# Kernel optimization log

Hardware: AMD Instinct MI355X
Metric: run time of the kernel (lower is better)

The kernel has to match this reference:

```python
import jax, jax.numpy as jnp
import numpy as np

INPUT_SIZE = 512
HIDDEN_SIZE = 512


def setup_inputs() -> dict:
    key = jax.random.key(0)
    k1, k2, k3, k4, k5 = jax.random.split(key, 5)
    B, N = 8, 2048
    x = jax.random.normal(k1, (B, N, INPUT_SIZE), dtype=jnp.float32)
    # Linear params (torch nn.Linear: y = x @ W^T + b), init scale ~ 1/sqrt(fan_in)
    s = 1.0 / np.sqrt(INPUT_SIZE)
    Wq = jax.random.uniform(k2, (HIDDEN_SIZE, INPUT_SIZE), minval=-s, maxval=s, dtype=jnp.float32)
    bq = jax.random.uniform(k3, (HIDDEN_SIZE,), minval=-s, maxval=s, dtype=jnp.float32)
    Wk = jax.random.uniform(k4, (HIDDEN_SIZE, INPUT_SIZE), minval=-s, maxval=s, dtype=jnp.float32)
    bk = jax.random.uniform(k5, (HIDDEN_SIZE,), minval=-s, maxval=s, dtype=jnp.float32)
    return {"x": x, "Wq": Wq, "bq": bq, "Wk": Wk, "bk": bk}


def reference(x, Wq, bq, Wk, bk):
    # q, k: [B, N, H]
    q = jnp.einsum('bnd,hd->bnh', x, Wq) + bq
    k = jnp.einsum('bnd,hd->bnh', x, Wk) + bk
    # scores: [B, N, N], softmax over last axis (dim=2)
    scores = jnp.einsum('bnh,bmh->bnm', q, k) / jnp.sqrt(jnp.float32(HIDDEN_SIZE))
    attn = jax.nn.softmax(scores, axis=2)
    # attended = attn^T @ x : [B, N, input_size]; squeeze(2) no-op since input_size>1
    attended = jnp.einsum('bnm,bnd->bmd', attn, x)
    return attended
```

## Files before the change

kernel.cpp:

```cpp
#include <hip/hip_runtime.h>

typedef __bf16 bf16x8 __attribute__((ext_vector_type(8)));
typedef __bf16 bf16x4 __attribute__((ext_vector_type(4)));
typedef float f32x4 __attribute__((ext_vector_type(4)));

__device__ __forceinline__ void async_copy16(const void* g, void* l) {
    __builtin_amdgcn_global_load_lds(
        (const __attribute__((address_space(1))) void*)g,
        (__attribute__((address_space(3))) void*)l, 16, 0, 0);
}

__global__ __launch_bounds__(256) void cvt_kernel(
    const float4* __restrict__ x, const float4* __restrict__ Wq,
    const float4* __restrict__ Wk, const float4* __restrict__ bq,
    const float4* __restrict__ bk,
    bf16x4* __restrict__ xb, bf16x4* __restrict__ Wb,
    float4* __restrict__ biasc) {
    int i = blockIdx.x * 256 + threadIdx.x;
    if (i < 2097152) {
        float4 v = x[i];
        bf16x4 r = {(__bf16)v.x, (__bf16)v.y, (__bf16)v.z, (__bf16)v.w};
        xb[i] = r;
    }
    if (i < 131072) {
        float4 v = (i < 65536) ? Wq[i] : Wk[i - 65536];
        bf16x4 r = {(__bf16)v.x, (__bf16)v.y, (__bf16)v.z, (__bf16)v.w};
        Wb[i] = r;
    }
    if (i < 256) {
        biasc[i] = (i < 128) ? bq[i] : bk[i - 128];
    }
}

__global__ __launch_bounds__(256) void fold_kernel(
    const __bf16* __restrict__ xb, const float* __restrict__ Z,
    ushort* __restrict__ xzT) {
    __shared__ float tile[64][65];
    __shared__ float zin[64];
    const int b = blockIdx.y;
    const int td = blockIdx.x & 7;
    const int tn = blockIdx.x >> 3;
    const int n0 = tn * 64, d0 = td * 64;
    const int t = threadIdx.x;
    if (t < 64) zin[t] = 1.0f / Z[b * 2048 + n0 + t];
    __syncthreads();
    const int cl = t & 15, c4 = cl * 4, rr = t >> 4;
#pragma unroll
    for (int j = 0; j < 4; ++j) {
        int nr = rr + j * 16;
        bf16x4 v = *(const bf16x4*)&xb[((size_t)b * 2048 + n0 + nr) * 512 + d0 + c4];
        tile[nr][c4 + 0] = (float)v[0];
        tile[nr][c4 + 1] = (float)v[1];
        tile[nr][c4 + 2] = (float)v[2];
        tile[nr][c4 + 3] = (float)v[3];
    }
    __syncthreads();
#pragma unroll
    for (int j2 = 0; j2 < 4; ++j2) {
        int dr = rr + j2 * 16;
        bf16x4 pk;
#pragma unroll
        for (int j = 0; j < 4; ++j)
            pk[j] = (__bf16)(tile[j * 16 + cl][dr] * zin[c4 + j]);
        *(bf16x4*)&xzT[((size_t)b * 512 + d0 + dr) * 2048 + n0 + c4] = pk;
    }
}

template <int EPI>
__global__ __launch_bounds__(256) void gemm_bt(
    const ushort* __restrict__ A, int lda, long sA,
    const ushort* __restrict__ B, int ldb, long sB,
    void* __restrict__ C, int ldc, long sC,
    int tiles_n, int K,
    const float* __restrict__ bias, float scale,
    float* __restrict__ Z, long sZ) {
    __shared__ ushort lA[128 * 64];
    __shared__ ushort lB[128 * 64];
    const int b = blockIdx.y;
    A += (size_t)b * sA;
    B += (size_t)b * sB;
    const int tm = blockIdx.x / tiles_n, tn = blockIdx.x % tiles_n;
    const int t = threadIdx.x;
    const int l = t & 63, w = t >> 6;
    const int wr = w >> 1, wc = w & 1;

    f32x4 acc[4][4];
#pragma unroll
    for (int i = 0; i < 4; ++i)
#pragma unroll
        for (int j = 0; j < 4; ++j) acc[i][j] = (f32x4){0.f, 0.f, 0.f, 0.f};

    for (int k0 = 0; k0 < K; k0 += 64) {
#pragma unroll
        for (int p = 0; p < 4; ++p) {
            int off = p * 4096 + t * 16;
            int row = off >> 7;
            int kb = off & 127;
            int kswz = kb ^ ((row & 7) << 4);
            async_copy16(A + (size_t)(tm * 128 + row) * lda + k0 + (kswz >> 1),
                         (char*)lA + off);
            async_copy16(B + (size_t)(tn * 128 + row) * ldb + k0 + (kswz >> 1),
                         (char*)lB + off);
        }
        __syncthreads();
#pragma unroll
        for (int ks = 0; ks < 2; ++ks) {
            bf16x8 af[4], bfr[4];
#pragma unroll
            for (int i = 0; i < 4; ++i) {
                int row = wr * 64 + i * 16 + (l & 15);
                int colb = (ks * 64 + (l >> 4) * 16) ^ ((row & 7) << 4);
                af[i] = *(const bf16x8*)((const char*)lA + row * 128 + colb);
            }
#pragma unroll
            for (int j = 0; j < 4; ++j) {
                int row = wc * 64 + j * 16 + (l & 15);
                int colb = (ks * 64 + (l >> 4) * 16) ^ ((row & 7) << 4);
                bfr[j] = *(const bf16x8*)((const char*)lB + row * 128 + colb);
            }
#pragma unroll
            for (int i = 0; i < 4; ++i)
#pragma unroll
                for (int j = 0; j < 4; ++j)
                    acc[i][j] = __builtin_amdgcn_mfma_f32_16x16x32_bf16(
                        af[i], bfr[j], acc[i][j], 0, 0, 0);
        }
        __syncthreads();
    }

    const int mb = tm * 128 + wr * 64;
    const int nb = tn * 128 + wc * 64;
    const int cl = l & 15;

    if (EPI == 0) {
        ushort* Cp = (ushort*)C + (size_t)b * sC;
#pragma unroll
        for (int i = 0; i < 4; ++i)
#pragma unroll
            for (int q = 0; q < 4; ++q) {
                int row = mb + i * 16 + (l >> 4) * 4 + q;
                bf16x4 pk;
#pragma unroll
                for (int j = 0; j < 4; ++j)
                    pk[j] = (__bf16)(acc[i][j][q] + bias[nb + j * 16 + cl]);
                *(bf16x4*)&Cp[(size_t)row * ldc + nb + cl * 4] = pk;
            }
    } else if (EPI == 1) {
        ushort* Cp = (ushort*)C + (size_t)b * sC;
        float colsum[4] = {0.f, 0.f, 0.f, 0.f};
#pragma unroll
        for (int i = 0; i < 4; ++i)
#pragma unroll
            for (int q = 0; q < 4; ++q) {
                int row = mb + i * 16 + (l >> 4) * 4 + q;
                bf16x4 pk;
#pragma unroll
                for (int j = 0; j < 4; ++j) {
                    float e = __expf(acc[i][j][q] * scale);
                    colsum[j] += e;
                    pk[j] = (__bf16)e;
                }
                *(bf16x4*)&Cp[(size_t)row * ldc + nb + cl * 4] = pk;
            }
#pragma unroll
        for (int j = 0; j < 4; ++j) {
            float s = colsum[j];
            s += __shfl_xor(s, 16);
            s += __shfl_xor(s, 32);
            if (l < 16) atomicAdd(&Z[b * sZ + nb + l * 4 + j], s);
        }
    } else {
        float* Cp = (float*)C + (size_t)b * sC;
#pragma unroll
        for (int i = 0; i < 4; ++i)
#pragma unroll
            for (int j = 0; j < 4; ++j)
#pragma unroll
                for (int q = 0; q < 4; ++q) {
                    int row = mb + i * 16 + (l >> 4) * 4 + q;
                    int col = nb + j * 16 + cl;
                    Cp[(size_t)row * ldc + col] = acc[i][j][q];
                }
    }
}

extern "C" void kernel_launch(void* const* d_in, const int* in_sizes, int n_in,
                              void* d_out, int out_size, void* d_ws, size_t ws_size,
                              hipStream_t stream) {
    const float* x  = (const float*)d_in[0];
    const float* Wq = (const float*)d_in[1];
    const float* bq = (const float*)d_in[2];
    const float* Wk = (const float*)d_in[3];
    const float* bk = (const float*)d_in[4];

    char* ws = (char*)d_ws;
    ushort* xb    = (ushort*)(ws);
    ushort* Wb    = (ushort*)(ws + 16777216);
    float*  biasc = (float*) (ws + 17825792);
    float*  Z     = (float*) (ws + 17829888);
    ushort* qkb   = (ushort*)(ws + 17895424);
    ushort* E     = (ushort*)(ws + 51449856);
    ushort* xzT   = qkb;

    hipMemsetAsync(Z, 0, 16384 * 4, stream);

    cvt_kernel<<<8192, 256, 0, stream>>>(
        (const float4*)x, (const float4*)Wq, (const float4*)Wk,
        (const float4*)bq, (const float4*)bk,
        (bf16x4*)xb, (bf16x4*)Wb, (float4*)biasc);

    gemm_bt<0><<<dim3(1024, 1), 256, 0, stream>>>(
        xb, 512, 0L, Wb, 512, 0L, qkb, 1024, 0L,
        8, 512, biasc, 0.f, nullptr, 0L);

    gemm_bt<1><<<dim3(256, 8), 256, 0, stream>>>(
        qkb + 512, 1024, 2048L * 1024, qkb, 1024, 2048L * 1024,
        E, 2048, 2048L * 2048, 16, 512,
        nullptr, 0.04419417382415922f, Z, 2048L);

    fold_kernel<<<dim3(256, 8), 256, 0, stream>>>((const __bf16*)xb, Z, xzT);

    gemm_bt<2><<<dim3(64, 8), 256, 0, stream>>>(
        E, 2048, 2048L * 2048, xzT, 2048, 512L * 2048,
        d_out, 512, 2048L * 512, 4, 2048,
        nullptr, 0.f, nullptr, 0L);
}
```

Measured before the change: 154.8 us.

## Use 256x128 tiles for projection and score GEMMs, add XCD swizzle and exp2

The projection and score GEMMs now use a taller 256x128 block tile, with 8x4 MFMA accumulators per wave, to raise arithmetic intensity and halve the grid. Block indices are remapped so consecutive tiles land on the same XCD, which should improve L2 reuse; the output GEMM gets the same remap. The score exponent uses exp2 with the scale folded in as log2e/sqrt(H). The larger tile doubles accumulator registers and LDS for A, which may lower occupancy, and a smaller grid may underfill the GPU.

```diff
diff --git a/kernel.cpp b/kernel.cpp
--- a/kernel.cpp
+++ b/kernel.cpp
@@ -10,7 +10,11 @@
         (__attribute__((address_space(3))) void*)l, 16, 0, 0);
 }
 
-__global__ __launch_bounds__(256) void cvt_kernel(
+__device__ __forceinline__ int xcd_swz(int bx, int nx) {
+    return (bx & 7) * (nx >> 3) + (bx >> 3);
+}
+
+__global__ __launch_bounds__(256) void k_cvt(
     const float4* __restrict__ x, const float4* __restrict__ Wq,
     const float4* __restrict__ Wk, const float4* __restrict__ bq,
     const float4* __restrict__ bk,
@@ -32,7 +36,7 @@
     }
 }
 
-__global__ __launch_bounds__(256) void fold_kernel(
+__global__ __launch_bounds__(256) void k_fold(
     const __bf16* __restrict__ xb, const float* __restrict__ Z,
     ushort* __restrict__ xzT) {
     __shared__ float tile[64][65];
@@ -67,19 +71,145 @@
 }
 
 template <int EPI>
-__global__ __launch_bounds__(256) void gemm_bt(
+__device__ __forceinline__ void gemm_fat_body(
     const ushort* __restrict__ A, int lda, long sA,
     const ushort* __restrict__ B, int ldb, long sB,
-    void* __restrict__ C, int ldc, long sC,
+    ushort* __restrict__ C, int ldc, long sC,
     int tiles_n, int K,
-    const float* __restrict__ bias, float scale,
+    const float* __restrict__ bias, float scale2,
     float* __restrict__ Z, long sZ) {
-    __shared__ ushort lA[128 * 64];
+    __shared__ ushort lA[256 * 64];
     __shared__ ushort lB[128 * 64];
     const int b = blockIdx.y;
     A += (size_t)b * sA;
     B += (size_t)b * sB;
-    const int tm = blockIdx.x / tiles_n, tn = blockIdx.x % tiles_n;
+    const int bx = xcd_swz(blockIdx.x, gridDim.x);
+    const int tm = bx / tiles_n, tn = bx % tiles_n;
+    const int t = threadIdx.x;
+    const int l = t & 63, w = t >> 6;
+    const int wr = w >> 1, wc = w & 1;
+
+    f32x4 acc[8][4];
+#pragma unroll
+    for (int i = 0; i < 8; ++i)
+#pragma unroll
+        for (int j = 0; j < 4; ++j) acc[i][j] = (f32x4){0.f, 0.f, 0.f, 0.f};
+
+    const int soff = t * 16;
+    const int skb = soff & 127;
+
+    for (int k0 = 0; k0 < K; k0 += 64) {
+#pragma unroll
+        for (int p = 0; p < 8; ++p) {
+            int off = p * 4096 + soff;
+            int row = off >> 7;
+            int kswz = skb ^ ((row & 7) << 4);
+            async_copy16(A + (size_t)(tm * 256 + row) * lda + k0 + (kswz >> 1),
+                         (char*)lA + off);
+        }
+#pragma unroll
+        for (int p = 0; p < 4; ++p) {
+            int off = p * 4096 + soff;
+            int row = off >> 7;
+            int kswz = skb ^ ((row & 7) << 4);
+            async_copy16(B + (size_t)(tn * 128 + row) * ldb + k0 + (kswz >> 1),
+                         (char*)lB + off);
+        }
+        __syncthreads();
+#pragma unroll
+        for (int ks = 0; ks < 2; ++ks) {
+            bf16x8 af[8], bfr[4];
+#pragma unroll
+            for (int i = 0; i < 8; ++i) {
+                int row = wr * 128 + i * 16 + (l & 15);
+                int colb = (ks * 64 + (l >> 4) * 16) ^ ((row & 7) << 4);
+                af[i] = *(const bf16x8*)((const char*)lA + row * 128 + colb);
+            }
+#pragma unroll
+            for (int j = 0; j < 4; ++j) {
+                int row = wc * 64 + j * 16 + (l & 15);
+                int colb = (ks * 64 + (l >> 4) * 16) ^ ((row & 7) << 4);
+                bfr[j] = *(const bf16x8*)((const char*)lB + row * 128 + colb);
+            }
+#pragma unroll
+            for (int i = 0; i < 8; ++i)
+#pragma unroll
+                for (int j = 0; j < 4; ++j)
+                    acc[i][j] = __builtin_amdgcn_mfma_f32_16x16x32_bf16(
+                        af[i], bfr[j], acc[i][j], 0, 0, 0);
+        }
+        __syncthreads();
+    }
+
+    const int mb = tm * 256 + wr * 128;
+    const int nb = tn * 128 + wc * 64;
+    const int cl = l & 15;
+    ushort* Cp = C + (size_t)b * sC;
+
+    if (EPI == 0) {
+#pragma unroll
+        for (int i = 0; i < 8; ++i)
+#pragma unroll
+            for (int q = 0; q < 4; ++q) {
+                int row = mb + i * 16 + (l >> 4) * 4 + q;
+                bf16x4 pk;
+#pragma unroll
+                for (int j = 0; j < 4; ++j)
+                    pk[j] = (__bf16)(acc[i][j][q] + bias[nb + j * 16 + cl]);
+                *(bf16x4*)&Cp[(size_t)row * ldc + nb + cl * 4] = pk;
+            }
+    } else {
+        float colsum[4] = {0.f, 0.f, 0.f, 0.f};
+#pragma unroll
+        for (int i = 0; i < 8; ++i)
+#pragma unroll
+            for (int q = 0; q < 4; ++q) {
+                int row = mb + i * 16 + (l >> 4) * 4 + q;
+                bf16x4 pk;
+#pragma unroll
+                for (int j = 0; j < 4; ++j) {
+                    float e = __builtin_amdgcn_exp2f(acc[i][j][q] * scale2);
+                    colsum[j] += e;
+                    pk[j] = (__bf16)e;
+                }
+                *(bf16x4*)&Cp[(size_t)row * ldc + nb + cl * 4] = pk;
+            }
+#pragma unroll
+        for (int j = 0; j < 4; ++j) {
+            float s = colsum[j];
+            s += __shfl_xor(s, 16);
+            s += __shfl_xor(s, 32);
+            if (l < 16) atomicAdd(&Z[b * sZ + nb + l * 4 + j], s);
+        }
+    }
+}
+
+__global__ __launch_bounds__(256) void k_proj(
+    const ushort* __restrict__ A, const ushort* __restrict__ B,
+    ushort* __restrict__ C, const float* __restrict__ bias) {
+    gemm_fat_body<0>(A, 512, 0L, B, 512, 0L, C, 1024, 0L,
+                     8, 512, bias, 0.f, nullptr, 0L);
+}
+
+__global__ __launch_bounds__(256) void k_escore(
+    const ushort* __restrict__ A, const ushort* __restrict__ B,
+    ushort* __restrict__ C, float* __restrict__ Z) {
+    gemm_fat_body<1>(A, 1024, 2048L * 1024, B, 1024, 2048L * 1024,
+                     C, 2048, 2048L * 2048, 16, 512,
+                     nullptr, 0.063758716f, Z, 2048L);
+}
+
+__global__ __launch_bounds__(256) void k_out(
+    const ushort* __restrict__ A, const ushort* __restrict__ B,
+    float* __restrict__ C) {
+    __shared__ ushort lA[128 * 64];
+    __shared__ ushort lB[128 * 64];
+    const int lda = 2048, ldb = 2048, ldc = 512, tiles_n = 4, K = 2048;
+    const int b = blockIdx.y;
+    A += (size_t)b * 2048L * 2048;
+    B += (size_t)b * 512L * 2048;
+    const int bx = xcd_swz(blockIdx.x, gridDim.x);
+    const int tm = bx / tiles_n, tn = bx % tiles_n;
     const int t = threadIdx.x;
     const int l = t & 63, w = t >> 6;
     const int wr = w >> 1, wc = w & 1;
@@ -130,58 +260,17 @@
 
     const int mb = tm * 128 + wr * 64;
     const int nb = tn * 128 + wc * 64;
-    const int cl = l & 15;
-
-    if (EPI == 0) {
-        ushort* Cp = (ushort*)C + (size_t)b * sC;
-#pragma unroll
-        for (int i = 0; i < 4; ++i)
+    float* Cp = C + (size_t)b * 2048L * 512;
+#pragma unroll
+    for (int i = 0; i < 4; ++i)
+#pragma unroll
+        for (int j = 0; j < 4; ++j)
 #pragma unroll
             for (int q = 0; q < 4; ++q) {
                 int row = mb + i * 16 + (l >> 4) * 4 + q;
-                bf16x4 pk;
-#pragma unroll
-                for (int j = 0; j < 4; ++j)
-                    pk[j] = (__bf16)(acc[i][j][q] + bias[nb + j * 16 + cl]);
-                *(bf16x4*)&Cp[(size_t)row * ldc + nb + cl * 4] = pk;
-            }
-    } else if (EPI == 1) {
-        ushort* Cp = (ushort*)C + (size_t)b * sC;
-        float colsum[4] = {0.f, 0.f, 0.f, 0.f};
-#pragma unroll
-        for (int i = 0; i < 4; ++i)
-#pragma unroll
-            for (int q = 0; q < 4; ++q) {
-                int row = mb + i * 16 + (l >> 4) * 4 + q;
-                bf16x4 pk;
-#pragma unroll
-                for (int j = 0; j < 4; ++j) {
-                    float e = __expf(acc[i][j][q] * scale);
-                    colsum[j] += e;
-                    pk[j] = (__bf16)e;
-                }
-                *(bf16x4*)&Cp[(size_t)row * ldc + nb + cl * 4] = pk;
-            }
-#pragma unroll
-        for (int j = 0; j < 4; ++j) {
-            float s = colsum[j];
-            s += __shfl_xor(s, 16);
-            s += __shfl_xor(s, 32);
-            if (l < 16) atomicAdd(&Z[b * sZ + nb + l * 4 + j], s);
-        }
-    } else {
-        float* Cp = (float*)C + (size_t)b * sC;
-#pragma unroll
-        for (int i = 0; i < 4; ++i)
-#pragma unroll
-            for (int j = 0; j < 4; ++j)
-#pragma unroll
-                for (int q = 0; q < 4; ++q) {
-                    int row = mb + i * 16 + (l >> 4) * 4 + q;
-                    int col = nb + j * 16 + cl;
-                    Cp[(size_t)row * ldc + col] = acc[i][j][q];
-                }
-    }
+                int col = nb + j * 16 + (l & 15);
+                Cp[(size_t)row * ldc + col] = acc[i][j][q];
+            }
 }
 
 extern "C" void kernel_launch(void* const* d_in, const int* in_sizes, int n_in,
@@ -202,26 +291,18 @@
     ushort* E     = (ushort*)(ws + 51449856);
     ushort* xzT   = qkb;
 
-    hipMemsetAsync(Z, 0, 16384 * 4, stream);
-
-    cvt_kernel<<<8192, 256, 0, stream>>>(
+    (void)hipMemsetAsync(Z, 0, 16384 * 4, stream);
+
+    k_cvt<<<8192, 256, 0, stream>>>(
         (const float4*)x, (const float4*)Wq, (const float4*)Wk,
         (const float4*)bq, (const float4*)bk,
         (bf16x4*)xb, (bf16x4*)Wb, (float4*)biasc);
 
-    gemm_bt<0><<<dim3(1024, 1), 256, 0, stream>>>(
-        xb, 512, 0L, Wb, 512, 0L, qkb, 1024, 0L,
-        8, 512, biasc, 0.f, nullptr, 0L);
-
-    gemm_bt<1><<<dim3(256, 8), 256, 0, stream>>>(
-        qkb + 512, 1024, 2048L * 1024, qkb, 1024, 2048L * 1024,
-        E, 2048, 2048L * 2048, 16, 512,
-        nullptr, 0.04419417382415922f, Z, 2048L);
-
-    fold_kernel<<<dim3(256, 8), 256, 0, stream>>>((const __bf16*)xb, Z, xzT);
-
-    gemm_bt<2><<<dim3(64, 8), 256, 0, stream>>>(
-        E, 2048, 2048L * 2048, xzT, 2048, 512L * 2048,
-        d_out, 512, 2048L * 512, 4, 2048,
-        nullptr, 0.f, nullptr, 0L);
-}
+    k_proj<<<dim3(512, 1), 256, 0, stream>>>(xb, Wb, qkb, biasc);
+
+    k_escore<<<dim3(128, 8), 256, 0, stream>>>(qkb + 512, qkb, E, Z);
+
+    k_fold<<<dim3(256, 8), 256, 0, stream>>>((const __bf16*)xb, Z, xzT);
+
+    k_out<<<dim3(64, 8), 256, 0, stream>>>(E, xzT, (float*)d_out);
+}
```

Result: slower. 173.0 us (+11.7%).

## Double-buffer GEMM LDS tiles with async prefetch, XCD swizzle, exp2 softmax

Applied to the files above, without the earlier changes.

Rewrites the shared GEMM core to double-buffer the LDS tiles. The tile for step k+2 is prefetched with async global-to-LDS copies while MFMAs run on the current tile, using manual vmcnt waits and raw barriers in place of two __syncthreads per iteration. It also remaps block indices so neighbouring tiles land on the same XCD, raises wave priority around the MFMA block, and replaces __expf with exp2 using a pre-scaled log2e constant. LDS use doubles to 64KB per block, which may reduce occupancy, and the hand-placed waitcnt and barrier logic adds risk of synchronisation errors.

```diff
diff --git a/kernel.cpp b/kernel.cpp
--- a/kernel.cpp
+++ b/kernel.cpp
@@ -10,7 +10,11 @@
         (__attribute__((address_space(3))) void*)l, 16, 0, 0);
 }
 
-__global__ __launch_bounds__(256) void cvt_kernel(
+__device__ __forceinline__ int xcd_swz(int bx, int nx) {
+    return (bx & 7) * (nx >> 3) + (bx >> 3);
+}
+
+__global__ __launch_bounds__(256) void k_cvt(
     const float4* __restrict__ x, const float4* __restrict__ Wq,
     const float4* __restrict__ Wk, const float4* __restrict__ bq,
     const float4* __restrict__ bk,
@@ -32,7 +36,7 @@
     }
 }
 
-__global__ __launch_bounds__(256) void fold_kernel(
+__global__ __launch_bounds__(256) void k_fold(
     const __bf16* __restrict__ xb, const float* __restrict__ Z,
     ushort* __restrict__ xzT) {
     __shared__ float tile[64][65];
@@ -67,65 +71,93 @@
 }
 
 template <int EPI>
-__global__ __launch_bounds__(256) void gemm_bt(
+__device__ __forceinline__ void gemm_core(
     const ushort* __restrict__ A, int lda, long sA,
     const ushort* __restrict__ B, int ldb, long sB,
     void* __restrict__ C, int ldc, long sC,
     int tiles_n, int K,
-    const float* __restrict__ bias, float scale,
+    const float* __restrict__ bias, float scale2,
     float* __restrict__ Z, long sZ) {
-    __shared__ ushort lA[128 * 64];
-    __shared__ ushort lB[128 * 64];
+    __shared__ ushort lA[2][8192];
+    __shared__ ushort lB[2][8192];
     const int b = blockIdx.y;
     A += (size_t)b * sA;
     B += (size_t)b * sB;
-    const int tm = blockIdx.x / tiles_n, tn = blockIdx.x % tiles_n;
+    const int bx = xcd_swz(blockIdx.x, gridDim.x);
+    const int tm = bx / tiles_n, tn = bx % tiles_n;
     const int t = threadIdx.x;
     const int l = t & 63, w = t >> 6;
     const int wr = w >> 1, wc = w & 1;
 
+    size_t gA[4], gB[4];
+    int dOf[4];
+#pragma unroll
+    for (int p = 0; p < 4; ++p) {
+        int off = p * 4096 + t * 16;
+        int row = off >> 7, kb = off & 127;
+        int kswz = kb ^ ((row & 7) << 4);
+        gA[p] = (size_t)(tm * 128 + row) * lda + (kswz >> 1);
+        gB[p] = (size_t)(tn * 128 + row) * ldb + (kswz >> 1);
+        dOf[p] = off;
+    }
+    auto stage = [&](int buf, int k0) {
+#pragma unroll
+        for (int p = 0; p < 4; ++p) {
+            async_copy16(A + gA[p] + k0, (char*)lA[buf] + dOf[p]);
+            async_copy16(B + gB[p] + k0, (char*)lB[buf] + dOf[p]);
+        }
+    };
+
     f32x4 acc[4][4];
 #pragma unroll
     for (int i = 0; i < 4; ++i)
 #pragma unroll
         for (int j = 0; j < 4; ++j) acc[i][j] = (f32x4){0.f, 0.f, 0.f, 0.f};
 
-    for (int k0 = 0; k0 < K; k0 += 64) {
-#pragma unroll
-        for (int p = 0; p < 4; ++p) {
-            int off = p * 4096 + t * 16;
-            int row = off >> 7;
-            int kb = off & 127;
-            int kswz = kb ^ ((row & 7) << 4);
-            async_copy16(A + (size_t)(tm * 128 + row) * lda + k0 + (kswz >> 1),
-                         (char*)lA + off);
-            async_copy16(B + (size_t)(tn * 128 + row) * ldb + k0 + (kswz >> 1),
-                         (char*)lB + off);
-        }
-        __syncthreads();
-#pragma unroll
-        for (int ks = 0; ks < 2; ++ks) {
-            bf16x8 af[4], bfr[4];
+    const int nk = K >> 6;
+    stage(0, 0);
+    stage(1, 64);
+    asm volatile("s_waitcnt vmcnt(8)" ::: "memory");
+    __builtin_amdgcn_s_barrier();
+    asm volatile("" ::: "memory");
+
+    for (int kt = 0; kt < nk; ++kt) {
+        const int cur = kt & 1;
+        bf16x8 af[4][2], bg[4][2];
+#pragma unroll
+        for (int ks = 0; ks < 2; ++ks)
 #pragma unroll
             for (int i = 0; i < 4; ++i) {
-                int row = wr * 64 + i * 16 + (l & 15);
-                int colb = (ks * 64 + (l >> 4) * 16) ^ ((row & 7) << 4);
-                af[i] = *(const bf16x8*)((const char*)lA + row * 128 + colb);
+                int rowA = wr * 64 + i * 16 + (l & 15);
+                int colA = (ks * 64 + (l >> 4) * 16) ^ ((rowA & 7) << 4);
+                af[i][ks] = *(const bf16x8*)((const char*)lA[cur] + rowA * 128 + colA);
+                int rowB = wc * 64 + i * 16 + (l & 15);
+                int colB = (ks * 64 + (l >> 4) * 16) ^ ((rowB & 7) << 4);
+                bg[i][ks] = *(const bf16x8*)((const char*)lB[cur] + rowB * 128 + colB);
             }
-#pragma unroll
-            for (int j = 0; j < 4; ++j) {
-                int row = wc * 64 + j * 16 + (l & 15);
-                int colb = (ks * 64 + (l >> 4) * 16) ^ ((row & 7) << 4);
-                bfr[j] = *(const bf16x8*)((const char*)lB + row * 128 + colb);
-            }
+        asm volatile("s_waitcnt lgkmcnt(0)" ::: "memory");
+        __builtin_amdgcn_sched_barrier(0);
+        __builtin_amdgcn_s_barrier();
+        asm volatile("" ::: "memory");
+        if (kt + 2 < nk) stage(cur, (kt + 2) << 6);
+        __builtin_amdgcn_sched_barrier(0);
+        __builtin_amdgcn_s_setprio(1);
+#pragma unroll
+        for (int ks = 0; ks < 2; ++ks)
 #pragma unroll
             for (int i = 0; i < 4; ++i)
 #pragma unroll
                 for (int j = 0; j < 4; ++j)
                     acc[i][j] = __builtin_amdgcn_mfma_f32_16x16x32_bf16(
-                        af[i], bfr[j], acc[i][j], 0, 0, 0);
+                        af[i][ks], bg[j][ks], acc[i][j], 0, 0, 0);
+        __builtin_amdgcn_s_setprio(0);
+        if (kt + 2 < nk) {
+            asm volatile("s_waitcnt vmcnt(8)" ::: "memory");
+        } else {
+            asm volatile("s_waitcnt vmcnt(0)" ::: "memory");
         }
-        __syncthreads();
+        __builtin_amdgcn_s_barrier();
+        asm volatile("" ::: "memory");
     }
 
     const int mb = tm * 128 + wr * 64;
@@ -156,7 +188,7 @@
                 bf16x4 pk;
 #pragma unroll
                 for (int j = 0; j < 4; ++j) {
-                    float e = __expf(acc[i][j][q] * scale);
+                    float e = __builtin_amdgcn_exp2f(acc[i][j][q] * scale2);
                     colsum[j] += e;
                     pk[j] = (__bf16)e;
                 }
@@ -184,6 +216,29 @@
     }
 }
 
+__global__ __launch_bounds__(256) void k_proj(
+    const ushort* __restrict__ A, const ushort* __restrict__ B,
+    ushort* __restrict__ C, const float* __restrict__ bias) {
+    gemm_core<0>(A, 512, 0L, B, 512, 0L, C, 1024, 0L,
+                 8, 512, bias, 0.f, nullptr, 0L);
+}
+
+__global__ __launch_bounds__(256) void k_escore(
+    const ushort* __restrict__ A, const ushort* __restrict__ B,
+    ushort* __restrict__ C, float* __restrict__ Z) {
+    gemm_core<1>(A, 1024, 2048L * 1024, B, 1024, 2048L * 1024,
+                 C, 2048, 2048L * 2048, 16, 512,
+                 nullptr, 0.063758716f, Z, 2048L);
+}
+
+__global__ __launch_bounds__(256) void k_out(
+    const ushort* __restrict__ A, const ushort* __restrict__ B,
+    float* __restrict__ C) {
+    gemm_core<2>(A, 2048, 2048L * 2048, B, 2048, 512L * 2048,
+                 C, 512, 2048L * 512, 4, 2048,
+                 nullptr, 0.f, nullptr, 0L);
+}
+
 extern "C" void kernel_launch(void* const* d_in, const int* in_sizes, int n_in,
                               void* d_out, int out_size, void* d_ws, size_t ws_size,
                               hipStream_t stream) {
@@ -202,26 +257,18 @@
     ushort* E     = (ushort*)(ws + 51449856);
     ushort* xzT   = qkb;
 
-    hipMemsetAsync(Z, 0, 16384 * 4, stream);
-
-    cvt_kernel<<<8192, 256, 0, stream>>>(
+    (void)hipMemsetAsync(Z, 0, 16384 * 4, stream);
+
+    k_cvt<<<8192, 256, 0, stream>>>(
         (const float4*)x, (const float4*)Wq, (const float4*)Wk,
         (const float4*)bq, (const float4*)bk,
         (bf16x4*)xb, (bf16x4*)Wb, (float4*)biasc);
 
-    gemm_bt<0><<<dim3(1024, 1), 256, 0, stream>>>(
-        xb, 512, 0L, Wb, 512, 0L, qkb, 1024, 0L,
-        8, 512, biasc, 0.f, nullptr, 0L);
-
-    gemm_bt<1><<<dim3(256, 8), 256, 0, stream>>>(
-        qkb + 512, 1024, 2048L * 1024, qkb, 1024, 2048L * 1024,
-        E, 2048, 2048L * 2048, 16, 512,
-        nullptr, 0.04419417382415922f, Z, 2048L);
-
-    fold_kernel<<<dim3(256, 8), 256, 0, stream>>>((const __bf16*)xb, Z, xzT);
-
-    gemm_bt<2><<<dim3(64, 8), 256, 0, stream>>>(
-        E, 2048, 2048L * 2048, xzT, 2048, 512L * 2048,
-        d_out, 512, 2048L * 512, 4, 2048,
-        nullptr, 0.f, nullptr, 0L);
-}
+    k_proj<<<dim3(1024, 1), 256, 0, stream>>>(xb, Wb, qkb, biasc);
+
+    k_escore<<<dim3(256, 8), 256, 0, stream>>>(qkb + 512, qkb, E, Z);
+
+    k_fold<<<dim3(256, 8), 256, 0, stream>>>((const __bf16*)xb, Z, xzT);
+
+    k_out<<<dim3(64, 8), 256, 0, stream>>>(E, xzT, (float*)d_out);
+}
```

New measurement: 132.6 us. -14.4%, faster.
